# Performance work log

Hardware: AMD Instinct MI355X
Metric: run time of the kernel (lower is better)

The kernel has to match this reference:

```python
import math
import jax, jax.numpy as jnp
import numpy as np

L, H, E, D = 12, 12, 768, 64   # stack_size, mh_size, embedding_dim, dim_w_matrices
B, S = 4, 512
EPS = 1e-5


def positional_enc(seq_len, model_dim):
    # faithful: power_ind = 10000 XOR int(2*i/dim)
    i = np.arange(model_dim)
    p = np.bitwise_xor(10000, (2 * i) // model_dim).astype(np.float32)
    pos = np.arange(seq_len, dtype=np.float32)[:, None]
    ang = pos / p[None, :]
    pe = np.where(i % 2 == 0, np.sin(ang), np.cos(ang)).astype(np.float32)
    return jnp.asarray(pe)


def layer_norm(x, g, b):
    mu = jnp.mean(x, axis=-1, keepdims=True)
    var = jnp.mean(jnp.square(x - mu), axis=-1, keepdims=True)
    return (x - mu) * jax.lax.rsqrt(var + EPS) * g + b


def encoder(x, wq, wo, g1, b1, fw, fb, g2, b2):
    # x: [B,S,E]; wq: [H,E,D]; wo: [E,H*D]; fw: [E,E] (torch Linear layout)
    bs = x.shape[0] * x.shape[1]
    nb = x.reshape(bs, E)                              # flatten batch (faithful)
    q = jnp.einsum('ne,hed->hnd', nb, wq)              # q == k == v (bug kept)
    scores = jax.nn.softmax(jnp.einsum('hnd,hmd->hnm', q, q) / math.sqrt(D), axis=-1)
    z = jnp.einsum('hnm,hmd->hnd', scores, q)          # [H,BS,D]
    zc = z.reshape(H * D, bs)                          # per-head view(D,-1) + cat
    mh = (wo @ zc).reshape(x.shape)                    # [B,S,E]
    l1 = layer_norm(x + mh, g1, b1)
    ffn = l1 @ fw.T + fb
    return layer_norm(l1 + ffn, g2, b2)


def setup_inputs() -> dict:
    key = jax.random.key(0)
    ks = jax.random.split(key, 8)

    def xavier(k, shape, fan_in, fan_out):
        lim = math.sqrt(6.0 / (fan_in + fan_out))
        return jax.random.uniform(k, shape, jnp.float32, -lim, lim)

    return {
        'tokens': jax.random.normal(ks[0], (B, S, E), jnp.float32),
        'wq':    xavier(ks[1], (L, H, E, D), E, D),
        'wo':    xavier(ks[2], (L, E, H * D), E, H * D),
        'ln1_g': jnp.ones((L, E), jnp.float32),
        'ln1_b': jnp.zeros((L, E), jnp.float32),
        'ffn_w': xavier(ks[3], (L, E, E), E, E),
        'ffn_b': jnp.zeros((L, E), jnp.float32),
        'ln2_g': jnp.ones((L, E), jnp.float32),
        'ln2_b': jnp.zeros((L, E), jnp.float32),
    }


def reference(tokens, wq, wo, ln1_g, ln1_b, ffn_w, ffn_b, ln2_g, ln2_b):
    pe = positional_enc(tokens.shape[1], tokens.shape[2])
    # faithful: layer 0 applied once on pe+tokens, then ALL layers (0 again) in loop
    x = encoder(pe + tokens, wq[0], wo[0], ln1_g[0], ln1_b[0],
                ffn_w[0], ffn_b[0], ln2_g[0], ln2_b[0])
    for l in range(L):
        x = encoder(x, wq[l], wo[l], ln1_g[l], ln1_b[l],
                    ffn_w[l], ffn_b[l], ln2_g[l], ln2_b[l])
    return x
```

## Files before the change

kernel.cpp:

```cpp
#include <hip/hip_runtime.h>
#include <hip/hip_bf16.h>


#define BS_TOK 2048
#define EMB 768
#define NH 12
#define HD 64
#define WQN (12 * NH * EMB * HD)

typedef __attribute__((ext_vector_type(8))) short bf16x8;
typedef __attribute__((ext_vector_type(4))) short bf16x4;
typedef __attribute__((ext_vector_type(4))) float f32x4;

__device__ __forceinline__ short f2bf(float f) {
  union { __hip_bfloat16 h; short s; } u;
  u.h = __float2bfloat16(f);
  return u.s;
}

#define MFMA16(a, b, c) __builtin_amdgcn_mfma_f32_16x16x32_bf16(a, b, c, 0, 0, 0)
#define SW64(r, k) ((r) * 64 + ((((k) >> 3) ^ ((r) & 7)) << 3) + ((k) & 7))
#define BAR() asm volatile("s_waitcnt lgkmcnt(0)\n\ts_barrier" ::: "memory")

__global__ __launch_bounds__(256) void cvt_weights_kernel(const float* __restrict__ wo,
                                                          const float* __restrict__ fw,
                                                          short* __restrict__ wob,
                                                          short* __restrict__ fwb) {
  const float* src = blockIdx.y ? fw : wo;
  short* dst = blockIdx.y ? fwb : wob;
  int i = (blockIdx.x * 256 + threadIdx.x) * 8;
  float4 a = *(const float4*)(src + i);
  float4 b = *(const float4*)(src + i + 4);
  bf16x8 t;
  t[0] = f2bf(a.x); t[1] = f2bf(a.y); t[2] = f2bf(a.z); t[3] = f2bf(a.w);
  t[4] = f2bf(b.x); t[5] = f2bf(b.y); t[6] = f2bf(b.z); t[7] = f2bf(b.w);
  *(bf16x8*)(dst + i) = t;
}

__global__ __launch_bounds__(256) void wq_trans_kernel(const float* __restrict__ wq,
                                                       short* __restrict__ wqT) {
  __shared__ short T[64 * 64];
  const int et = blockIdx.x;
  const int lh = blockIdx.y;
  const int tid = threadIdx.x;
  const float* src = wq + ((size_t)lh * EMB + et * 64) * HD;
  {
    int r = tid >> 2, c16 = (tid & 3) << 4;
    const float* p = src + r * HD + c16;
    float4 x0 = *(const float4*)(p + 0);
    float4 x1 = *(const float4*)(p + 4);
    float4 x2 = *(const float4*)(p + 8);
    float4 x3 = *(const float4*)(p + 12);
    bf16x8 a, b;
    a[0] = f2bf(x0.x); a[1] = f2bf(x0.y); a[2] = f2bf(x0.z); a[3] = f2bf(x0.w);
    a[4] = f2bf(x1.x); a[5] = f2bf(x1.y); a[6] = f2bf(x1.z); a[7] = f2bf(x1.w);
    b[0] = f2bf(x2.x); b[1] = f2bf(x2.y); b[2] = f2bf(x2.z); b[3] = f2bf(x2.w);
    b[4] = f2bf(x3.x); b[5] = f2bf(x3.y); b[6] = f2bf(x3.z); b[7] = f2bf(x3.w);
    int g = c16 >> 3;
    *(bf16x8*)&T[r * 64 + ((g ^ (r & 7)) << 3)] = a;
    *(bf16x8*)&T[r * 64 + (((g + 1) ^ (r & 7)) << 3)] = b;
  }
  __syncthreads();
  {
    int d = tid >> 2, e16 = (tid & 3) << 4;
    bf16x8 t0, t1;
#pragma unroll
    for (int j = 0; j < 8; ++j) t0[j] = T[SW64(e16 + j, d)];
#pragma unroll
    for (int j = 0; j < 8; ++j) t1[j] = T[SW64(e16 + 8 + j, d)];
    short* q = wqT + ((size_t)lh * HD + d) * EMB + et * 64 + e16;
    *(bf16x8*)(q) = t0;
    *(bf16x8*)(q + 8) = t1;
  }
}

__global__ __launch_bounds__(256) void pe_add_kernel(const float* __restrict__ tok,
                                                     float* __restrict__ X,
                                                     short* __restrict__ Xb) {
  int idx = blockIdx.x * 256 + threadIdx.x;
  int e = idx % EMB;
  int t = idx / EMB;
  int s = t & 511;
  float p = (e < 384) ? 10000.0f : 10001.0f;
  float ang = (float)s / p;
  float pe = (e & 1) ? cosf(ang) : sinf(ang);
  float v = tok[idx] + pe;
  X[idx] = v;
  Xb[idx] = f2bf(v);
}

__device__ __forceinline__ void load64(const short* __restrict__ src, int ld,
                                       int row0, int k0, bf16x8* r, int tid) {
  int rr = tid >> 2, kb = (tid & 3) << 4;
  const short* p = src + (size_t)(row0 + rr) * ld + k0 + kb;
  r[0] = *(const bf16x8*)(p);
  r[1] = *(const bf16x8*)(p + 8);
}
__device__ __forceinline__ void write64(short* dst, const bf16x8* r, int tid) {
  int rr = tid >> 2, g = (tid & 3) << 1;
  *(bf16x8*)&dst[rr * 64 + (((g + 0) ^ (rr & 7)) << 3)] = r[0];
  *(bf16x8*)&dst[rr * 64 + (((g + 1) ^ (rr & 7)) << 3)] = r[1];
}

__device__ __forceinline__ void load128(const short* __restrict__ src, int ld,
                                        int row0, int k0, bf16x8* r, int tid) {
  int rr = tid >> 1, kb = (tid & 1) << 5;
  const short* p = src + (size_t)(row0 + rr) * ld + k0 + kb;
  r[0] = *(const bf16x8*)(p);
  r[1] = *(const bf16x8*)(p + 8);
  r[2] = *(const bf16x8*)(p + 16);
  r[3] = *(const bf16x8*)(p + 24);
}
__device__ __forceinline__ void write128(short* dst, const bf16x8* r, int tid) {
  int rr = tid >> 1, g = (tid & 1) << 2;
#pragma unroll
  for (int i = 0; i < 4; ++i)
    *(bf16x8*)&dst[rr * 64 + (((g + i) ^ (rr & 7)) << 3)] = r[i];
}

__device__ __forceinline__ void load_zc(const short* __restrict__ Zcb,
                                        int k0, int col0, bf16x8 cr[2], int tid) {
  int kk = tid >> 2, nb = (tid & 3) << 4;
  const short* p = Zcb + (size_t)(k0 + kk) * BS_TOK + col0 + nb;
  cr[0] = *(const bf16x8*)(p);
  cr[1] = *(const bf16x8*)(p + 8);
}
__device__ __forceinline__ void write_zc(short* dst, const bf16x8 cr[2], int tid) {
  int kk = tid >> 2, nb = (tid & 3) << 4;
#pragma unroll
  for (int j = 0; j < 8; ++j) dst[SW64(nb + j, kk)] = cr[0][j];
#pragma unroll
  for (int j = 0; j < 8; ++j) dst[SW64(nb + 8 + j, kk)] = cr[1][j];
}

#define GEMM_TILE_COMPUTE(As, Bs, acc)                                              \
  {                                                                                 \
    _Pragma("unroll") for (int s = 0; s < 2; ++s) {                                 \
      int ra = (w << 4) + l15;                                                      \
      bf16x8 af = *(const bf16x8*)&As[ra * 64 + ((((s << 2) + quad) ^ (ra & 7)) << 3)]; \
      _Pragma("unroll") for (int nt = 0; nt < 4; ++nt) {                            \
        int rb = (nt << 4) + l15;                                                   \
        bf16x8 bf = *(const bf16x8*)&Bs[rb * 64 + ((((s << 2) + quad) ^ (rb & 7)) << 3)]; \
        acc[nt] = MFMA16(af, bf, acc[nt]);                                          \
      }                                                                             \
    }                                                                               \
  }

#define GEMM_TILE_COMPUTE2(As, Bs, acc)                                             \
  {                                                                                 \
    _Pragma("unroll") for (int s = 0; s < 2; ++s) {                                 \
      bf16x8 af[2];                                                                 \
      _Pragma("unroll") for (int u = 0; u < 2; ++u) {                               \
        int ra = (w << 5) + (u << 4) + l15;                                         \
        af[u] = *(const bf16x8*)&As[ra * 64 + ((((s << 2) + quad) ^ (ra & 7)) << 3)]; \
      }                                                                             \
      _Pragma("unroll") for (int nt = 0; nt < 4; ++nt) {                            \
        int rb = (nt << 4) + l15;                                                   \
        bf16x8 bf = *(const bf16x8*)&Bs[rb * 64 + ((((s << 2) + quad) ^ (rb & 7)) << 3)]; \
        acc[0][nt] = MFMA16(af[0], bf, acc[0][nt]);                                 \
        acc[1][nt] = MFMA16(af[1], bf, acc[1][nt]);                                 \
      }                                                                             \
    }                                                                               \
  }

__global__ __launch_bounds__(256) void gemm_q_kernel(const short* __restrict__ Xb,
                                                     const short* __restrict__ WqT,
                                                     short* __restrict__ Qo,
                                                     short* __restrict__ Qt) {
  __shared__ short As[2][64 * 64];
  __shared__ short Bs[2][64 * 64];
  const int m0 = blockIdx.x * 64;
  const int h = blockIdx.y;
  const int tid = threadIdx.x;
  const int w = tid >> 6, lane = tid & 63, l15 = lane & 15, quad = lane >> 4;
  const short* wqh = WqT + (size_t)h * (HD * EMB);
  f32x4 acc[4] = {};
  bf16x8 ar[2], br[2];
  load64(Xb, EMB, m0, 0, ar, tid);
  load64(wqh, EMB, 0, 0, br, tid);
  write64(As[0], ar, tid);
  write64(Bs[0], br, tid);
  load64(Xb, EMB, m0, 64, ar, tid);
  load64(wqh, EMB, 0, 64, br, tid);
  BAR();
  for (int k0 = 0; k0 < EMB; k0 += 64) {
    const int cur = (k0 >> 6) & 1;
    const short* Ac = As[cur];
    const short* Bc = Bs[cur];
    GEMM_TILE_COMPUTE(Ac, Bc, acc);
    if (k0 + 64 < EMB) {
      write64((short*)As[cur ^ 1], ar, tid);
      write64((short*)Bs[cur ^ 1], br, tid);
      if (k0 + 128 < EMB) {
        load64(Xb, EMB, m0, k0 + 128, ar, tid);
        load64(wqh, EMB, 0, k0 + 128, br, tid);
      }
    }
    BAR();
  }
  short* T = (short*)As[0];
#pragma unroll
  for (int nt = 0; nt < 4; ++nt)
#pragma unroll
    for (int r = 0; r < 4; ++r)
      T[SW64((w << 4) + (quad << 2) + r, (nt << 4) + l15)] = f2bf(acc[nt][r]);
  __syncthreads();
  {
    int r2 = tid >> 2, kb = (tid & 3) << 4;
    int g = kb >> 3;
    bf16x8 q0v = *(const bf16x8*)&T[r2 * 64 + ((g ^ (r2 & 7)) << 3)];
    bf16x8 q1v = *(const bf16x8*)&T[r2 * 64 + (((g + 1) ^ (r2 & 7)) << 3)];
    short* qo = Qo + (size_t)h * (BS_TOK * HD) + (size_t)(m0 + r2) * HD + kb;
    *(bf16x8*)(qo) = q0v;
    *(bf16x8*)(qo + 8) = q1v;
  }
  {
    int d = tid >> 2, tok0 = (tid & 3) << 4;
    bf16x8 t0, t1;
#pragma unroll
    for (int j = 0; j < 8; ++j) t0[j] = T[SW64(tok0 + j, d)];
#pragma unroll
    for (int j = 0; j < 8; ++j) t1[j] = T[SW64(tok0 + 8 + j, d)];
    short* qt = Qt + (size_t)h * (HD * BS_TOK) + (size_t)d * BS_TOK + m0 + tok0;
    *(bf16x8*)(qt) = t0;
    *(bf16x8*)(qt + 8) = t1;
  }
}

__device__ __forceinline__ void attn_tile(const short* __restrict__ K_,
                                          const short* __restrict__ V_,
                                          short* __restrict__ P_,
                                          const bf16x8 qf[2], f32x4 o[4],
                                          float& lpl, int l15, int quad) {
  f32x4 s[4];
  __builtin_amdgcn_s_setprio(1);
#pragma unroll
  for (int ct = 0; ct < 4; ++ct) {
    f32x4 a = (f32x4){0.f, 0.f, 0.f, 0.f};
#pragma unroll
    for (int ks = 0; ks < 2; ++ks) {
      int row = ct * 16 + l15;
      int c = ks * 4 + quad;
      bf16x8 kf = *(const bf16x8*)(&K_[row * 64 + ((c ^ (row & 7)) << 3)]);
      a = MFMA16(kf, qf[ks], a);
    }
    s[ct] = a;
  }
  __builtin_amdgcn_s_setprio(0);
#pragma unroll
  for (int ct = 0; ct < 4; ++ct) {
    bf16x4 pv4;
    float pp[4];
#pragma unroll
    for (int r = 0; r < 4; ++r) {
      pp[r] = exp2f(s[ct][r] * 0.18033688011112042f);
      pv4[r] = f2bf(pp[r]);
    }
    lpl += (pp[0] + pp[1]) + (pp[2] + pp[3]);
    int g = 2 * ct + (quad >> 1);
    *(bf16x4*)&P_[l15 * 64 + ((g ^ (l15 & 7)) << 3) + ((quad & 1) << 2)] = pv4;
  }
  __builtin_amdgcn_s_setprio(1);
#pragma unroll
  for (int ks = 0; ks < 2; ++ks) {
    int c = ks * 4 + quad;
    bf16x8 pf = *(const bf16x8*)(&P_[l15 * 64 + ((c ^ (l15 & 7)) << 3)]);
#pragma unroll
    for (int dt = 0; dt < 4; ++dt) {
      int row = dt * 16 + l15;
      bf16x8 vf = *(const bf16x8*)(&V_[row * 64 + ((c ^ (row & 7)) << 3)]);
      o[dt] = MFMA16(pf, vf, o[dt]);
    }
  }
  __builtin_amdgcn_s_setprio(0);
}

__global__ __launch_bounds__(256) void attn_mfma_kernel(const short* __restrict__ Q,
                                                        const short* __restrict__ Qt,
                                                        short* __restrict__ Zcb) {
  __shared__ short Ks[4][64 * 64];
  __shared__ short Vt[4][64 * 64];
  __shared__ short Pw[4][2][16 * 64];
  const int h = blockIdx.y;
  const int q0 = blockIdx.x * 64;
  const int tid = threadIdx.x;
  const int lane = tid & 63;
  const int wv = tid >> 6;
  const int l15 = lane & 15;
  const int quad = lane >> 4;
  const short* Qh = Q + (size_t)h * (BS_TOK * HD);
  const short* Qth = Qt + (size_t)h * (HD * BS_TOK);
  short* myP0 = Pw[wv][0];
  short* myP1 = Pw[wv][1];

  bf16x8 qf[2];
  {
    const short* qp = Qh + (size_t)(q0 + wv * 16 + l15) * HD + quad * 8;
    qf[0] = *(const bf16x8*)(qp);
    qf[1] = *(const bf16x8*)(qp + 32);
  }

  f32x4 o[4] = {};
  float lpl = 0.f;

  bf16x8 kreg[2][2], vreg[2][2];
#pragma unroll
  for (int t = 0; t < 2; ++t)
#pragma unroll
    for (int i = 0; i < 2; ++i) {
      int c = i * 256 + tid;
      kreg[t][i] = *(const bf16x8*)(Qh + (size_t)t * 4096 + c * 8);
      vreg[t][i] = *(const bf16x8*)(Qth + (size_t)(c >> 3) * BS_TOK + t * 64 + (c & 7) * 8);
    }
#pragma unroll
  for (int t = 0; t < 2; ++t)
#pragma unroll
    for (int i = 0; i < 2; ++i) {
      int c = i * 256 + tid, row = c >> 3, g = c & 7;
      *(bf16x8*)&Ks[t][row * 64 + ((g ^ (row & 7)) << 3)] = kreg[t][i];
      *(bf16x8*)&Vt[t][row * 64 + ((g ^ (row & 7)) << 3)] = vreg[t][i];
    }
#pragma unroll
  for (int t = 0; t < 2; ++t)
#pragma unroll
    for (int i = 0; i < 2; ++i) {
      int c = i * 256 + tid;
      kreg[t][i] = *(const bf16x8*)(Qh + (size_t)(2 + t) * 4096 + c * 8);
      vreg[t][i] = *(const bf16x8*)(Qth + (size_t)(c >> 3) * BS_TOK + (2 + t) * 64 + (c & 7) * 8);
    }
  BAR();

  for (int p = 0; p < 16; ++p) {
    const int base = (p & 1) * 2;
    if (p + 1 < 16) {
      const int nb = ((p + 1) & 1) * 2;
#pragma unroll
      for (int t = 0; t < 2; ++t)
#pragma unroll
        for (int i = 0; i < 2; ++i) {
          int c = i * 256 + tid, row = c >> 3, g = c & 7;
          *(bf16x8*)&Ks[nb + t][row * 64 + ((g ^ (row & 7)) << 3)] = kreg[t][i];
          *(bf16x8*)&Vt[nb + t][row * 64 + ((g ^ (row & 7)) << 3)] = vreg[t][i];
        }
      if (p + 2 < 16) {
        int gt0 = (p + 2) * 2;
#pragma unroll
        for (int t = 0; t < 2; ++t)
#pragma unroll
          for (int i = 0; i < 2; ++i) {
            int c = i * 256 + tid;
            kreg[t][i] = *(const bf16x8*)(Qh + (size_t)(gt0 + t) * 4096 + c * 8);
            vreg[t][i] = *(const bf16x8*)(Qth + (size_t)(c >> 3) * BS_TOK + (gt0 + t) * 64 + (c & 7) * 8);
          }
      }
    }
    attn_tile(Ks[base], Vt[base], myP0, qf, o, lpl, l15, quad);
    attn_tile(Ks[base + 1], Vt[base + 1], myP1, qf, o, lpl, l15, quad);
    BAR();
  }

  lpl += __shfl_xor(lpl, 16, 64);
  lpl += __shfl_xor(lpl, 32, 64);

  float rl[4];
#pragma unroll
  for (int r = 0; r < 4; ++r)
    rl[r] = 1.0f / __shfl(lpl, quad * 4 + r, 64);

  short* T = (short*)Ks[0];
#pragma unroll
  for (int dt = 0; dt < 4; ++dt)
#pragma unroll
    for (int r = 0; r < 4; ++r)
      T[SW64(wv * 16 + quad * 4 + r, dt * 16 + l15)] = f2bf(o[dt][r] * rl[r]);
  __syncthreads();
  {
    short* zo = Zcb + (size_t)h * (BS_TOK * HD) + (size_t)q0 * HD;
    int r2 = tid >> 2, kb = (tid & 3) << 4;
    int g = kb >> 3;
    bf16x8 z0 = *(const bf16x8*)&T[r2 * 64 + ((g ^ (r2 & 7)) << 3)];
    bf16x8 z1 = *(const bf16x8*)&T[r2 * 64 + (((g + 1) ^ (r2 & 7)) << 3)];
    *(bf16x8*)(zo + r2 * 64 + kb) = z0;
    *(bf16x8*)(zo + r2 * 64 + kb + 8) = z1;
  }
}

__global__ __launch_bounds__(256) void gemm_out_kernel(const short* __restrict__ Wob,
                                                       const short* __restrict__ Zcb,
                                                       float* __restrict__ Pp) {
  __shared__ short As[2][128 * 64];
  __shared__ short Bs[2][64 * 64];
  const int n0 = blockIdx.x * 64;
  const int m0 = blockIdx.y * 128;
  const int kz = blockIdx.z * 384;
  const int tid = threadIdx.x;
  const int w = tid >> 6, lane = tid & 63, l15 = lane & 15, quad = lane >> 4;
  f32x4 acc[2][4] = {};
  bf16x8 ar[4], cr[2];
  load128(Wob, EMB, m0, kz, ar, tid);
  load_zc(Zcb, kz, n0, cr, tid);
  write128((short*)As[0], ar, tid);
  write_zc((short*)Bs[0], cr, tid);
  load128(Wob, EMB, m0, kz + 64, ar, tid);
  load_zc(Zcb, kz + 64, n0, cr, tid);
  BAR();
  for (int k0 = 0; k0 < 384; k0 += 64) {
    const int cur = (k0 >> 6) & 1;
    const short* Ac = As[cur];
    const short* Bc = Bs[cur];
    GEMM_TILE_COMPUTE2(Ac, Bc, acc);
    if (k0 + 64 < 384) {
      write128((short*)As[cur ^ 1], ar, tid);
      write_zc((short*)Bs[cur ^ 1], cr, tid);
      if (k0 + 128 < 384) {
        load128(Wob, EMB, m0, kz + k0 + 128, ar, tid);
        load_zc(Zcb, kz + k0 + 128, n0, cr, tid);
      }
    }
    BAR();
  }
  float* P = Pp + (size_t)blockIdx.z * (BS_TOK * EMB);
#pragma unroll
  for (int u = 0; u < 2; ++u)
#pragma unroll
    for (int nt = 0; nt < 4; ++nt)
#pragma unroll
      for (int r = 0; r < 4; ++r)
        P[(size_t)(m0 + (w << 5) + (u << 4) + (quad << 2) + r) * BS_TOK + n0 +
          (nt << 4) + l15] = acc[u][nt][r];
}

__global__ __launch_bounds__(256) void gemm_ffn_kernel(const short* __restrict__ L1b,
                                                       const short* __restrict__ Fwb,
                                                       const float* __restrict__ Fb,
                                                       float* __restrict__ Pp) {
  __shared__ short As[2][128 * 64];
  __shared__ short Bs[2][64 * 64];
  const int m0 = blockIdx.x * 128;
  const int n0 = blockIdx.y * 64;
  const int kz = blockIdx.z * 384;
  const int tid = threadIdx.x;
  const int w = tid >> 6, lane = tid & 63, l15 = lane & 15, quad = lane >> 4;
  f32x4 acc[2][4] = {};
  bf16x8 ar[4], br[2];
  load128(L1b, EMB, m0, kz, ar, tid);
  load64(Fwb, EMB, n0, kz, br, tid);
  write128((short*)As[0], ar, tid);
  write64((short*)Bs[0], br, tid);
  load128(L1b, EMB, m0, kz + 64, ar, tid);
  load64(Fwb, EMB, n0, kz + 64, br, tid);
  BAR();
  for (int k0 = 0; k0 < 384; k0 += 64) {
    const int cur = (k0 >> 6) & 1;
    const short* Ac = As[cur];
    const short* Bc = Bs[cur];
    GEMM_TILE_COMPUTE2(Ac, Bc, acc);
    if (k0 + 64 < 384) {
      write128((short*)As[cur ^ 1], ar, tid);
      write64((short*)Bs[cur ^ 1], br, tid);
      if (k0 + 128 < 384) {
        load128(L1b, EMB, m0, kz + k0 + 128, ar, tid);
        load64(Fwb, EMB, n0, kz + k0 + 128, br, tid);
      }
    }
    BAR();
  }
  float* P = Pp + (size_t)blockIdx.z * (BS_TOK * EMB);
  const bool addb = (blockIdx.z == 0);
#pragma unroll
  for (int nt = 0; nt < 4; ++nt) {
    float bias = addb ? Fb[n0 + (nt << 4) + l15] : 0.0f;
#pragma unroll
    for (int u = 0; u < 2; ++u)
#pragma unroll
      for (int r = 0; r < 4; ++r)
        P[(size_t)(m0 + (w << 5) + (u << 4) + (quad << 2) + r) * EMB + n0 +
          (nt << 4) + l15] = acc[u][nt][r] + bias;
  }
}

__global__ __launch_bounds__(256) void ln_kernel(const float* __restrict__ Xa,
                                                 const float* __restrict__ P,
                                                 const float* __restrict__ g,
                                                 const float* __restrict__ bb,
                                                 float* __restrict__ Out,
                                                 short* __restrict__ Outb) {
  const int NB = BS_TOK * EMB;
  const int wv = threadIdx.x >> 6, lane = threadIdx.x & 63;
  const int t = blockIdx.x * 4 + wv;
  const float* xa = Xa + (size_t)t * EMB;
  const float* p0 = P + (size_t)t * EMB;
  const float* p1 = p0 + NB;
  float4 v[3];
  float s = 0.f;
#pragma unroll
  for (int i = 0; i < 3; ++i) {
    int e = lane * 4 + i * 256;
    float4 a = *(const float4*)(xa + e);
    float4 b = *(const float4*)(p0 + e);
    float4 c = *(const float4*)(p1 + e);
    v[i].x = a.x + b.x + c.x;
    v[i].y = a.y + b.y + c.y;
    v[i].z = a.z + b.z + c.z;
    v[i].w = a.w + b.w + c.w;
    s += v[i].x + v[i].y + v[i].z + v[i].w;
  }
#pragma unroll
  for (int o = 32; o > 0; o >>= 1) s += __shfl_xor(s, o, 64);
  float mu = s * (1.0f / EMB);
  float q = 0.f;
#pragma unroll
  for (int i = 0; i < 3; ++i) {
    float dx = v[i].x - mu, dy = v[i].y - mu, dz = v[i].z - mu, dw = v[i].w - mu;
    q += dx * dx + dy * dy + dz * dz + dw * dw;
  }
#pragma unroll
  for (int o = 32; o > 0; o >>= 1) q += __shfl_xor(q, o, 64);
  float var = q * (1.0f / EMB);
  float r = rsqrtf(var + 1e-5f);
#pragma unroll
  for (int i = 0; i < 3; ++i) {
    int e = lane * 4 + i * 256;
    float4 gg = *(const float4*)(g + e);
    float4 bv = *(const float4*)(bb + e);
    float4 res;
    res.x = (v[i].x - mu) * r * gg.x + bv.x;
    res.y = (v[i].y - mu) * r * gg.y + bv.y;
    res.z = (v[i].z - mu) * r * gg.z + bv.z;
    res.w = (v[i].w - mu) * r * gg.w + bv.w;
    *(float4*)(Out + (size_t)t * EMB + e) = res;
    bf16x4 ob;
    ob[0] = f2bf(res.x);
    ob[1] = f2bf(res.y);
    ob[2] = f2bf(res.z);
    ob[3] = f2bf(res.w);
    *(bf16x4*)(Outb + (size_t)t * EMB + e) = ob;
  }
}

extern "C" void kernel_launch(void* const* d_in, const int* in_sizes, int n_in,
                              void* d_out, int out_size, void* d_ws, size_t ws_size,
                              hipStream_t stream) {
  const float* tok = (const float*)d_in[0];
  const float* wq = (const float*)d_in[1];
  const float* wo = (const float*)d_in[2];
  const float* g1 = (const float*)d_in[3];
  const float* b1 = (const float*)d_in[4];
  const float* fw = (const float*)d_in[5];
  const float* fb = (const float*)d_in[6];
  const float* g2 = (const float*)d_in[7];
  const float* b2 = (const float*)d_in[8];
  const int NB = BS_TOK * EMB;
  float* bufA = (float*)d_ws;
  float* bufB = bufA + NB;
  float* bufC = bufB + NB;
  float* bufD = bufC + NB;
  short* XbA = (short*)(bufD + NB);
  short* L1b = XbA + NB;
  short* Qbf = L1b + NB;
  short* Qtb = Qbf + NB;
  short* Zcb = Qtb + NB;
  short* wqTb = Zcb + NB;
  short* wob = wqTb + WQN;
  short* fwb = wob + WQN;

  cvt_weights_kernel<<<dim3(WQN / (256 * 8), 2), 256, 0, stream>>>(wo, fw, wob, fwb);
  wq_trans_kernel<<<dim3(12, 12 * NH), 256, 0, stream>>>(wq, wqTb);
  pe_add_kernel<<<NB / 256, 256, 0, stream>>>(tok, bufA, XbA);
  for (int it = 0; it < 13; ++it) {
    int l = (it == 0) ? 0 : it - 1;
    gemm_q_kernel<<<dim3(32, NH), 256, 0, stream>>>(
        XbA, wqTb + (size_t)l * (NH * HD * EMB), Qbf, Qtb);
    attn_mfma_kernel<<<dim3(32, NH), 256, 0, stream>>>(Qbf, Qtb, Zcb);
    gemm_out_kernel<<<dim3(32, 6, 2), 256, 0, stream>>>(
        wob + (size_t)l * (EMB * EMB), Zcb, bufB);
    ln_kernel<<<BS_TOK / 4, 256, 0, stream>>>(bufA, bufB, g1 + l * EMB, b1 + l * EMB,
                                              bufD, L1b);
    gemm_ffn_kernel<<<dim3(16, 12, 2), 256, 0, stream>>>(
        L1b, fwb + (size_t)l * (EMB * EMB), fb + l * EMB, bufB);
    float* ln2_dst = (it == 12) ? (float*)d_out : bufA;
    ln_kernel<<<BS_TOK / 4, 256, 0, stream>>>(bufD, bufB, g2 + l * EMB, b2 + l * EMB,
                                              ln2_dst, XbA);
  }
}
```

Before: 1.179 ms.

## Split attention keys across wave pairs and halve query tile per block

The attention kernel now handles 32 queries per block instead of 64. Its four waves form two pairs, and each pair processes half of the key sequence with its own single-buffered shared tile. Partial outputs and row sums are combined through shared memory before normalization, and the grid doubles to 64x12 blocks. Shared memory drops and launch bounds request 3 blocks per CU, so the intent is more blocks in flight and better occupancy. In exchange, each block does fewer tiles between barriers and pays an extra reduction step.

```diff
diff --git a/kernel.cpp b/kernel.cpp
--- a/kernel.cpp
+++ b/kernel.cpp
@@ -275,27 +275,28 @@
   __builtin_amdgcn_s_setprio(0);
 }
 
-__global__ __launch_bounds__(256) void attn_mfma_kernel(const short* __restrict__ Q,
-                                                        const short* __restrict__ Qt,
-                                                        short* __restrict__ Zcb) {
-  __shared__ short Ks[4][64 * 64];
-  __shared__ short Vt[4][64 * 64];
-  __shared__ short Pw[4][2][16 * 64];
+__global__ __launch_bounds__(256, 3) void attn_mfma_kernel(const short* __restrict__ Q,
+                                                           const short* __restrict__ Qt,
+                                                           short* __restrict__ Zcb) {
+  __shared__ short sm[20480];
   const int h = blockIdx.y;
-  const int q0 = blockIdx.x * 64;
+  const int q0 = blockIdx.x * 32;
   const int tid = threadIdx.x;
   const int lane = tid & 63;
   const int wv = tid >> 6;
+  const int wq = wv & 1;
+  const int hb = wv >> 1;
   const int l15 = lane & 15;
   const int quad = lane >> 4;
   const short* Qh = Q + (size_t)h * (BS_TOK * HD);
   const short* Qth = Qt + (size_t)h * (HD * BS_TOK);
-  short* myP0 = Pw[wv][0];
-  short* myP1 = Pw[wv][1];
+  short* Ksh = sm + hb * 4096;
+  short* Vth = sm + 8192 + hb * 4096;
+  short* myP = sm + 16384 + wv * 1024;
 
   bf16x8 qf[2];
   {
-    const short* qp = Qh + (size_t)(q0 + wv * 16 + l15) * HD + quad * 8;
+    const short* qp = Qh + (size_t)(q0 + wq * 16 + l15) * HD + quad * 8;
     qf[0] = *(const bf16x8*)(qp);
     qf[1] = *(const bf16x8*)(qp + 32);
   }
@@ -303,85 +304,89 @@
   f32x4 o[4] = {};
   float lpl = 0.f;
 
-  bf16x8 kreg[2][2], vreg[2][2];
-#pragma unroll
-  for (int t = 0; t < 2; ++t)
-#pragma unroll
-    for (int i = 0; i < 2; ++i) {
-      int c = i * 256 + tid;
-      kreg[t][i] = *(const bf16x8*)(Qh + (size_t)t * 4096 + c * 8);
-      vreg[t][i] = *(const bf16x8*)(Qth + (size_t)(c >> 3) * BS_TOK + t * 64 + (c & 7) * 8);
-    }
-#pragma unroll
-  for (int t = 0; t < 2; ++t)
-#pragma unroll
-    for (int i = 0; i < 2; ++i) {
-      int c = i * 256 + tid, row = c >> 3, g = c & 7;
-      *(bf16x8*)&Ks[t][row * 64 + ((g ^ (row & 7)) << 3)] = kreg[t][i];
-      *(bf16x8*)&Vt[t][row * 64 + ((g ^ (row & 7)) << 3)] = vreg[t][i];
-    }
-#pragma unroll
-  for (int t = 0; t < 2; ++t)
-#pragma unroll
-    for (int i = 0; i < 2; ++i) {
-      int c = i * 256 + tid;
-      kreg[t][i] = *(const bf16x8*)(Qh + (size_t)(2 + t) * 4096 + c * 8);
-      vreg[t][i] = *(const bf16x8*)(Qth + (size_t)(c >> 3) * BS_TOK + (2 + t) * 64 + (c & 7) * 8);
-    }
+  const int t128 = tid & 127;
+  bf16x8 kreg[4], vreg[4];
+#pragma unroll
+  for (int i = 0; i < 4; ++i) {
+    int c = i * 128 + t128;
+    kreg[i] = *(const bf16x8*)(Qh + (size_t)(hb * 16) * 4096 + c * 8);
+    vreg[i] = *(const bf16x8*)(Qth + (size_t)(c >> 3) * BS_TOK + (hb * 16) * 64 + (c & 7) * 8);
+  }
+#pragma unroll
+  for (int i = 0; i < 4; ++i) {
+    int c = i * 128 + t128, row = c >> 3, g = c & 7;
+    *(bf16x8*)&Ksh[row * 64 + ((g ^ (row & 7)) << 3)] = kreg[i];
+    *(bf16x8*)&Vth[row * 64 + ((g ^ (row & 7)) << 3)] = vreg[i];
+  }
+#pragma unroll
+  for (int i = 0; i < 4; ++i) {
+    int c = i * 128 + t128;
+    kreg[i] = *(const bf16x8*)(Qh + (size_t)(hb * 16 + 1) * 4096 + c * 8);
+    vreg[i] = *(const bf16x8*)(Qth + (size_t)(c >> 3) * BS_TOK + (hb * 16 + 1) * 64 + (c & 7) * 8);
+  }
   BAR();
 
-  for (int p = 0; p < 16; ++p) {
-    const int base = (p & 1) * 2;
-    if (p + 1 < 16) {
-      const int nb = ((p + 1) & 1) * 2;
-#pragma unroll
-      for (int t = 0; t < 2; ++t)
-#pragma unroll
-        for (int i = 0; i < 2; ++i) {
-          int c = i * 256 + tid, row = c >> 3, g = c & 7;
-          *(bf16x8*)&Ks[nb + t][row * 64 + ((g ^ (row & 7)) << 3)] = kreg[t][i];
-          *(bf16x8*)&Vt[nb + t][row * 64 + ((g ^ (row & 7)) << 3)] = vreg[t][i];
+  for (int t = 0; t < 16; ++t) {
+    attn_tile(Ksh, Vth, myP, qf, o, lpl, l15, quad);
+    BAR();
+    if (t + 1 < 16) {
+#pragma unroll
+      for (int i = 0; i < 4; ++i) {
+        int c = i * 128 + t128, row = c >> 3, g = c & 7;
+        *(bf16x8*)&Ksh[row * 64 + ((g ^ (row & 7)) << 3)] = kreg[i];
+        *(bf16x8*)&Vth[row * 64 + ((g ^ (row & 7)) << 3)] = vreg[i];
+      }
+      if (t + 2 < 16) {
+        int gt = hb * 16 + t + 2;
+#pragma unroll
+        for (int i = 0; i < 4; ++i) {
+          int c = i * 128 + t128;
+          kreg[i] = *(const bf16x8*)(Qh + (size_t)gt * 4096 + c * 8);
+          vreg[i] = *(const bf16x8*)(Qth + (size_t)(c >> 3) * BS_TOK + gt * 64 + (c & 7) * 8);
         }
-      if (p + 2 < 16) {
-        int gt0 = (p + 2) * 2;
-#pragma unroll
-        for (int t = 0; t < 2; ++t)
-#pragma unroll
-          for (int i = 0; i < 2; ++i) {
-            int c = i * 256 + tid;
-            kreg[t][i] = *(const bf16x8*)(Qh + (size_t)(gt0 + t) * 4096 + c * 8);
-            vreg[t][i] = *(const bf16x8*)(Qth + (size_t)(c >> 3) * BS_TOK + (gt0 + t) * 64 + (c & 7) * 8);
-          }
       }
     }
-    attn_tile(Ks[base], Vt[base], myP0, qf, o, lpl, l15, quad);
-    attn_tile(Ks[base + 1], Vt[base + 1], myP1, qf, o, lpl, l15, quad);
     BAR();
   }
 
   lpl += __shfl_xor(lpl, 16, 64);
   lpl += __shfl_xor(lpl, 32, 64);
 
-  float rl[4];
-#pragma unroll
-  for (int r = 0; r < 4; ++r)
-    rl[r] = 1.0f / __shfl(lpl, quad * 4 + r, 64);
-
-  short* T = (short*)Ks[0];
-#pragma unroll
-  for (int dt = 0; dt < 4; ++dt)
+  float* Fo = (float*)sm;
+  float* Fl = (float*)sm + 2048;
+  if (hb == 1) {
+#pragma unroll
+    for (int dt = 0; dt < 4; ++dt)
+#pragma unroll
+      for (int r = 0; r < 4; ++r)
+        Fo[(wq * 16 + quad * 4 + r) * 64 + dt * 16 + l15] = o[dt][r];
+    if (quad == 0) Fl[wq * 16 + l15] = lpl;
+  }
+  __syncthreads();
+  short* T = sm + 8192;
+  if (hb == 0) {
+#pragma unroll
+    for (int dt = 0; dt < 4; ++dt)
+#pragma unroll
+      for (int r = 0; r < 4; ++r)
+        o[dt][r] += Fo[(wq * 16 + quad * 4 + r) * 64 + dt * 16 + l15];
+    float ltot = lpl + Fl[wq * 16 + l15];
+    float rl[4];
 #pragma unroll
     for (int r = 0; r < 4; ++r)
-      T[SW64(wv * 16 + quad * 4 + r, dt * 16 + l15)] = f2bf(o[dt][r] * rl[r]);
+      rl[r] = 1.0f / __shfl(ltot, quad * 4 + r, 64);
+#pragma unroll
+    for (int dt = 0; dt < 4; ++dt)
+#pragma unroll
+      for (int r = 0; r < 4; ++r)
+        T[SW64(wq * 16 + quad * 4 + r, dt * 16 + l15)] = f2bf(o[dt][r] * rl[r]);
+  }
   __syncthreads();
   {
     short* zo = Zcb + (size_t)h * (BS_TOK * HD) + (size_t)q0 * HD;
-    int r2 = tid >> 2, kb = (tid & 3) << 4;
-    int g = kb >> 3;
-    bf16x8 z0 = *(const bf16x8*)&T[r2 * 64 + ((g ^ (r2 & 7)) << 3)];
-    bf16x8 z1 = *(const bf16x8*)&T[r2 * 64 + (((g + 1) ^ (r2 & 7)) << 3)];
-    *(bf16x8*)(zo + r2 * 64 + kb) = z0;
-    *(bf16x8*)(zo + r2 * 64 + kb + 8) = z1;
+    int r2 = tid >> 3, g = tid & 7;
+    bf16x8 z = *(const bf16x8*)&T[r2 * 64 + ((g ^ (r2 & 7)) << 3)];
+    *(bf16x8*)(zo + r2 * 64 + g * 8) = z;
   }
 }
 
@@ -571,7 +576,7 @@
     int l = (it == 0) ? 0 : it - 1;
     gemm_q_kernel<<<dim3(32, NH), 256, 0, stream>>>(
         XbA, wqTb + (size_t)l * (NH * HD * EMB), Qbf, Qtb);
-    attn_mfma_kernel<<<dim3(32, NH), 256, 0, stream>>>(Qbf, Qtb, Zcb);
+    attn_mfma_kernel<<<dim3(64, NH), 256, 0, stream>>>(Qbf, Qtb, Zcb);
     gemm_out_kernel<<<dim3(32, 6, 2), 256, 0, stream>>>(
         wob + (size_t)l * (EMB * EMB), Zcb, bufB);
     ln_kernel<<<BS_TOK / 4, 256, 0, stream>>>(bufA, bufB, g1 + l * EMB, b1 + l * EMB,
```

Result: faster. 1.111 ms (-5.7%).
